# Optimization experiments

Measured on AMD Instinct MI355X. Metric: run time of the kernel, lower is better.

The kernel has to match this reference:

```python
import jax, jax.numpy as jnp
import numpy as np

B, C_IMG, H, W = 16, 512, 32, 32
C_AUD, K_LEN, N_HEADS = 512, 256, 8
HEAD_DIM = C_AUD // N_HEADS
EPS = 1e-5


def setup_inputs() -> dict:
    key = jax.random.key(0)
    ks = jax.random.split(key, 12)
    s_img = 1.0 / np.sqrt(C_IMG)
    s_aud = 1.0 / np.sqrt(C_AUD)
    return {
        "img_feat": jax.random.normal(ks[0], (B, C_IMG, H, W), jnp.float32),
        "audio_feat": jax.random.normal(ks[1], (B, K_LEN, C_AUD), jnp.float32),
        "Wq": jax.random.uniform(ks[2], (C_IMG, C_AUD), jnp.float32, -s_img, s_img),
        "bq": jnp.zeros((C_AUD,), jnp.float32),
        "Wk": jax.random.uniform(ks[3], (C_AUD, C_AUD), jnp.float32, -s_aud, s_aud),
        "bk": jnp.zeros((C_AUD,), jnp.float32),
        "Wv": jax.random.uniform(ks[4], (C_AUD, C_AUD), jnp.float32, -s_aud, s_aud),
        "bv": jnp.zeros((C_AUD,), jnp.float32),
        "Wo": jax.random.uniform(ks[5], (C_AUD, C_IMG), jnp.float32, -s_aud, s_aud),
        "bo": jnp.zeros((C_IMG,), jnp.float32),
        "gamma": jnp.ones((C_IMG,), jnp.float32),
        "beta": jnp.zeros((C_IMG,), jnp.float32),
    }


def reference(img_feat, audio_feat, Wq, bq, Wk, bk, Wv, bv, Wo, bo, gamma, beta):
    b, c, h, w = img_feat.shape
    # b c h w -> b (h w) c
    img_seq = img_feat.reshape(b, c, h * w).transpose(0, 2, 1)
    q = img_seq @ Wq + bq                      # [b, q, C_AUD]
    k = audio_feat @ Wk + bk                   # [b, k, C_AUD]
    v = audio_feat @ Wv + bv
    # split heads: b s (h d) -> b h s d
    def split(x):
        bs, s, _ = x.shape
        return x.reshape(bs, s, N_HEADS, HEAD_DIM).transpose(0, 2, 1, 3)
    qh, kh, vh = split(q), split(k), split(v)
    scale = HEAD_DIM ** -0.5
    scores = jnp.einsum('bhqd,bhkd->bhqk', qh, kh) * scale
    weights = jax.nn.softmax(scores, axis=-1)
    attn = jnp.einsum('bhqk,bhkd->bhqd', weights, vh)
    attn = attn.transpose(0, 2, 1, 3).reshape(b, h * w, C_AUD)
    proj = attn @ Wo + bo                      # [b, q, C_IMG]
    y = img_seq + proj
    mu = jnp.mean(y, axis=-1, keepdims=True)
    var = jnp.mean((y - mu) ** 2, axis=-1, keepdims=True)
    y = (y - mu) * jax.lax.rsqrt(var + EPS) * gamma + beta
    # b (h w) c -> b c h w
    return y.transpose(0, 2, 1).reshape(b, c, h, w)
```

## Files before the change

### kernel.cpp

```cpp
#include <hip/hip_runtime.h>
#include <cstddef>

#define B_SZ 16
#define HW 1024
#define CCH 512
#define K_LEN 256
#define N_HEADS 8
#define EPS 1e-5f

typedef __bf16 bf16;
typedef bf16 bf16x8 __attribute__((ext_vector_type(8)));
typedef bf16 bf16x4 __attribute__((ext_vector_type(4)));
typedef bf16 bf16x2 __attribute__((ext_vector_type(2)));
typedef float f32x4 __attribute__((ext_vector_type(4)));

__device__ __forceinline__ void gl_lds16(const bf16* g, bf16* l) {
    __builtin_amdgcn_global_load_lds(
        (const __attribute__((address_space(1))) void*)g,
        (__attribute__((address_space(3))) void*)l, 16, 0, 0);
}

__global__ __launch_bounds__(256) void transpose_cast_img(
    const float* __restrict__ src, bf16* __restrict__ dst)
{
    const int b  = blockIdx.z;
    const int s0 = blockIdx.x * 64;
    const int c0 = blockIdx.y * 64;
    __shared__ bf16 T[64][72];
    const int tid = threadIdx.x;
    {
        const int r = tid >> 2, cs = (tid & 3) << 4;
        const float* sp = src + ((size_t)b * CCH + c0 + r) * HW + s0 + cs;
        #pragma unroll
        for (int i = 0; i < 4; ++i) {
            float4 f = *(const float4*)(sp + i * 4);
            T[r][cs + i*4 + 0] = (bf16)f.x;
            T[r][cs + i*4 + 1] = (bf16)f.y;
            T[r][cs + i*4 + 2] = (bf16)f.z;
            T[r][cs + i*4 + 3] = (bf16)f.w;
        }
    }
    __syncthreads();
    {
        const int ss = tid >> 2, ks = (tid & 3) << 4;
        bf16x8 a, b8;
        #pragma unroll
        for (int j = 0; j < 8; ++j) { a[j] = T[ks + j][ss]; b8[j] = T[ks + 8 + j][ss]; }
        bf16* dp = dst + ((size_t)b * HW + s0 + ss) * CCH + c0 + ks;
        *(bf16x8*)dp = a;
        *(bf16x8*)(dp + 8) = b8;
    }
}

__global__ __launch_bounds__(256) void transpose_cast_w(
    const float* __restrict__ Wq, const float* __restrict__ Wk,
    const float* __restrict__ Wv, const float* __restrict__ Wo,
    bf16* __restrict__ dst)
{
    const int w = blockIdx.z;
    const float* src = (w == 0) ? Wq : (w == 1) ? Wk : (w == 2) ? Wv : Wo;
    const int n0 = blockIdx.x * 64;
    const int k0 = blockIdx.y * 64;
    __shared__ bf16 T[64][72];
    const int tid = threadIdx.x;
    {
        const int r = tid >> 2, cs = (tid & 3) << 4;
        const float* sp = src + (size_t)(k0 + r) * CCH + n0 + cs;
        #pragma unroll
        for (int i = 0; i < 4; ++i) {
            float4 f = *(const float4*)(sp + i * 4);
            T[r][cs + i*4 + 0] = (bf16)f.x;
            T[r][cs + i*4 + 1] = (bf16)f.y;
            T[r][cs + i*4 + 2] = (bf16)f.z;
            T[r][cs + i*4 + 3] = (bf16)f.w;
        }
    }
    __syncthreads();
    {
        const int nn = tid >> 2, ks = (tid & 3) << 4;
        bf16x8 a, b8;
        #pragma unroll
        for (int j = 0; j < 8; ++j) { a[j] = T[ks + j][nn]; b8[j] = T[ks + 8 + j][nn]; }
        bf16* dp = dst + (size_t)w * CCH * CCH + (size_t)(n0 + nn) * CCH + k0 + ks;
        *(bf16x8*)dp = a;
        *(bf16x8*)(dp + 8) = b8;
    }
}

__global__ __launch_bounds__(256) void cast_audio(
    const float* __restrict__ src, bf16* __restrict__ dst)
{
    const size_t i = ((size_t)blockIdx.x * 256 + threadIdx.x) * 8;
    float4 a = *(const float4*)(src + i);
    float4 b = *(const float4*)(src + i + 4);
    bf16x8 o;
    o[0] = (bf16)a.x; o[1] = (bf16)a.y; o[2] = (bf16)a.z; o[3] = (bf16)a.w;
    o[4] = (bf16)b.x; o[5] = (bf16)b.y; o[6] = (bf16)b.z; o[7] = (bf16)b.w;
    *(bf16x8*)(dst + i) = o;
}

__global__ __launch_bounds__(256) void gemm_bf16_mfma(
    const bf16* __restrict__ A, const bf16* __restrict__ Bt,
    const float* __restrict__ bias, bf16* __restrict__ out)
{
    const int tid  = threadIdx.x;
    const int wave = tid >> 6, lane = tid & 63;
    const int m0 = blockIdx.x * 128;
    const int n0 = blockIdx.y * 128;
    const int l15 = lane & 15, quad = lane >> 4;
    const int wm = (wave >> 1) * 64, wn = (wave & 1) * 64;

    __shared__ bf16 As[128 * 32];
    __shared__ bf16 Bs[128 * 32];

    const int r16 = lane >> 2;
    const int ks  = (lane & 3) * 8;

    f32x4 acc[4][4];
    #pragma unroll
    for (int i = 0; i < 4; ++i)
        #pragma unroll
        for (int j = 0; j < 4; ++j)
            acc[i][j] = (f32x4){0.f, 0.f, 0.f, 0.f};

    for (int k0 = 0; k0 < 512; k0 += 32) {
        #pragma unroll
        for (int i = 0; i < 2; ++i) {
            const int c = wave * 2 + i;
            gl_lds16(A  + (size_t)(m0 + c * 16 + r16) * 512 + k0 + ks, &As[c * 512]);
            gl_lds16(Bt + (size_t)(n0 + c * 16 + r16) * 512 + k0 + ks, &Bs[c * 512]);
        }
        __syncthreads();
        bf16x8 af[4], bfr[4];
        #pragma unroll
        for (int i = 0; i < 4; ++i)
            af[i] = *(const bf16x8*)&As[(wm + i * 16 + l15) * 32 + quad * 8];
        #pragma unroll
        for (int j = 0; j < 4; ++j)
            bfr[j] = *(const bf16x8*)&Bs[(wn + j * 16 + l15) * 32 + quad * 8];
        #pragma unroll
        for (int i = 0; i < 4; ++i)
            #pragma unroll
            for (int j = 0; j < 4; ++j)
                acc[i][j] = __builtin_amdgcn_mfma_f32_16x16x32_bf16(bfr[j], af[i], acc[i][j], 0, 0, 0);
        __syncthreads();
    }

    #pragma unroll
    for (int j = 0; j < 4; ++j) {
        const int gn = n0 + wn + j * 16 + quad * 4;
        const f32x4 bv4 = *(const f32x4*)(bias + gn);
        #pragma unroll
        for (int i = 0; i < 4; ++i) {
            const int gm = m0 + wm + i * 16 + l15;
            bf16x4 ov;
            #pragma unroll
            for (int r = 0; r < 4; ++r) ov[r] = (bf16)(acc[i][j][r] + bv4[r]);
            *(bf16x4*)(out + (size_t)gm * 512 + gn) = ov;
        }
    }
}

__global__ __launch_bounds__(256) void gemm_kv_mfma(
    const bf16* __restrict__ A, const bf16* __restrict__ Bt,
    const float* __restrict__ bk, const float* __restrict__ bv,
    bf16* __restrict__ khout, bf16* __restrict__ vtout)
{
    const int tid  = threadIdx.x;
    const int wave = tid >> 6, lane = tid & 63;
    const int m0 = blockIdx.x * 128;
    const int n0 = blockIdx.y * 128;
    const int l15 = lane & 15, quad = lane >> 4;
    const int wm = (wave >> 1) * 64, wn = (wave & 1) * 64;

    __shared__ bf16 As[128 * 32];
    __shared__ bf16 Bs[128 * 32];

    const int r16 = lane >> 2;
    const int ks  = (lane & 3) * 8;

    f32x4 acc[4][4];
    #pragma unroll
    for (int i = 0; i < 4; ++i)
        #pragma unroll
        for (int j = 0; j < 4; ++j)
            acc[i][j] = (f32x4){0.f, 0.f, 0.f, 0.f};

    for (int k0 = 0; k0 < 512; k0 += 32) {
        #pragma unroll
        for (int i = 0; i < 2; ++i) {
            const int c = wave * 2 + i;
            gl_lds16(A  + (size_t)(m0 + c * 16 + r16) * 512 + k0 + ks, &As[c * 512]);
            gl_lds16(Bt + (size_t)(n0 + c * 16 + r16) * 512 + k0 + ks, &Bs[c * 512]);
        }
        __syncthreads();
        bf16x8 af[4], bfr[4];
        #pragma unroll
        for (int i = 0; i < 4; ++i)
            af[i] = *(const bf16x8*)&As[(wm + i * 16 + l15) * 32 + quad * 8];
        #pragma unroll
        for (int j = 0; j < 4; ++j)
            bfr[j] = *(const bf16x8*)&Bs[(wn + j * 16 + l15) * 32 + quad * 8];
        #pragma unroll
        for (int i = 0; i < 4; ++i)
            #pragma unroll
            for (int j = 0; j < 4; ++j)
                acc[i][j] = __builtin_amdgcn_mfma_f32_16x16x32_bf16(af[i], bfr[j], acc[i][j], 0, 0, 0);
        __syncthreads();
    }

    #pragma unroll
    for (int j = 0; j < 4; ++j) {
        const int gn = n0 + wn + j * 16 + l15;
        if (gn < 512) {
            const int h = gn >> 6, d = gn & 63;
            const float bias = bk[gn];
            #pragma unroll
            for (int i = 0; i < 4; ++i) {
                const int gm = m0 + wm + i * 16 + quad * 4;
                const int b = gm >> 8, key = gm & 255;
                bf16* base = khout + ((((size_t)b * N_HEADS + h) * K_LEN) + key) * 64 + d;
                #pragma unroll
                for (int r = 0; r < 4; ++r)
                    base[(size_t)r * 64] = (bf16)(acc[i][j][r] + bias);
            }
        } else {
            const int ch = gn - 512;
            const int h = ch >> 6, d = ch & 63;
            const float bias = bv[ch];
            #pragma unroll
            for (int i = 0; i < 4; ++i) {
                const int gm = m0 + wm + i * 16 + quad * 4;
                const int b = gm >> 8, key = gm & 255;
                bf16x4 pk;
                #pragma unroll
                for (int r = 0; r < 4; ++r) pk[r] = (bf16)(acc[i][j][r] + bias);
                *(bf16x4*)(vtout + (((size_t)b * N_HEADS + h) * 64 + d) * K_LEN + key) = pk;
            }
        }
    }
}

__global__ __launch_bounds__(256) void attn_mfma(
    const bf16* __restrict__ q,
    const bf16* __restrict__ kh,
    const bf16* __restrict__ vt,
    bf16* __restrict__ o)
{
    const int bh = blockIdx.x;
    const int s0 = blockIdx.y * 64;
    const int tid = threadIdx.x;
    const int wave = tid >> 6, lane = tid & 63;
    const int l15 = lane & 15, quad = lane >> 4;
    const int b = bh >> 3, h = bh & 7;

    __shared__ bf16 KsPt[18432];
    __shared__ bf16 Vs[16896];

    const bf16* khb = kh + (size_t)bh * K_LEN * 64;
    const bf16* vtb = vt + (size_t)bh * 64 * K_LEN;

    #pragma unroll
    for (int i = 0; i < 8; ++i) {
        const int chunk = tid + (i << 8);
        const int key = chunk >> 3, dseg = (chunk & 7) << 3;
        *(bf16x8*)&KsPt[key * 72 + dseg] = *(const bf16x8*)(khb + key * 64 + dseg);
        const int d = chunk >> 5, kseg = (chunk & 31) << 3;
        *(bf16x8*)&Vs[d * 264 + kseg] = *(const bf16x8*)(vtb + d * 256 + kseg);
    }
    __syncthreads();

    const int qrow = s0 + wave * 16 + l15;
    const bf16* qp = q + ((size_t)(b * HW + qrow)) * 512 + h * 64 + quad * 8;
    const bf16x8 qf0 = *(const bf16x8*)qp;
    const bf16x8 qf1 = *(const bf16x8*)(qp + 32);

    f32x4 acc[16];
    #pragma unroll
    for (int m = 0; m < 16; ++m) acc[m] = (f32x4){0.f, 0.f, 0.f, 0.f};
    #pragma unroll
    for (int m = 0; m < 16; ++m) {
        const bf16x8 a0 = *(const bf16x8*)&KsPt[(m * 16 + l15) * 72 + quad * 8];
        const bf16x8 a1 = *(const bf16x8*)&KsPt[(m * 16 + l15) * 72 + 32 + quad * 8];
        acc[m] = __builtin_amdgcn_mfma_f32_16x16x32_bf16(a0, qf0, acc[m], 0, 0, 0);
        acc[m] = __builtin_amdgcn_mfma_f32_16x16x32_bf16(a1, qf1, acc[m], 0, 0, 0);
    }

    float mx = -1e30f;
    #pragma unroll
    for (int m = 0; m < 16; ++m)
        mx = fmaxf(mx, fmaxf(fmaxf(acc[m][0], acc[m][1]), fmaxf(acc[m][2], acc[m][3])));
    mx = fmaxf(mx, __shfl_xor(mx, 16, 64));
    mx = fmaxf(mx, __shfl_xor(mx, 32, 64));

    __syncthreads();

    bf16* PtW = &KsPt[wave * 4224];
    float l_sum = 0.f;
    #pragma unroll
    for (int m = 0; m < 16; ++m) {
        bf16x4 pk;
        #pragma unroll
        for (int r = 0; r < 4; ++r) {
            const float p = __expf((acc[m][r] - mx) * 0.125f);
            l_sum += p;
            pk[r] = (bf16)p;
        }
        *(bf16x4*)&PtW[l15 * 264 + m * 16 + quad * 4] = pk;
    }
    l_sum += __shfl_xor(l_sum, 16, 64);
    l_sum += __shfl_xor(l_sum, 32, 64);
    __syncthreads();

    f32x4 oacc[4];
    #pragma unroll
    for (int m = 0; m < 4; ++m) oacc[m] = (f32x4){0.f, 0.f, 0.f, 0.f};
    #pragma unroll
    for (int s = 0; s < 8; ++s) {
        const bf16x8 pb = *(const bf16x8*)&PtW[l15 * 264 + s * 32 + quad * 8];
        #pragma unroll
        for (int m = 0; m < 4; ++m) {
            const bf16x8 va = *(const bf16x8*)&Vs[(m * 16 + l15) * 264 + s * 32 + quad * 8];
            oacc[m] = __builtin_amdgcn_mfma_f32_16x16x32_bf16(va, pb, oacc[m], 0, 0, 0);
        }
    }

    const float inv = 1.0f / l_sum;
    bf16* op = o + ((size_t)(b * HW + qrow)) * 512 + h * 64 + quad * 4;
    #pragma unroll
    for (int m = 0; m < 4; ++m) {
        bf16x4 ov;
        #pragma unroll
        for (int r = 0; r < 4; ++r) ov[r] = (bf16)(oacc[m][r] * inv);
        *(bf16x4*)&op[m * 16] = ov;
    }
}

__global__ __launch_bounds__(512) void gemm_oln(
    const bf16* __restrict__ A,
    const bf16* __restrict__ Wt,
    const float* __restrict__ bo,
    const bf16* __restrict__ imgb,
    const float* __restrict__ gamma, const float* __restrict__ beta,
    float* __restrict__ out)
{
    const int tid  = threadIdx.x;
    const int wave = tid >> 6, lane = tid & 63;
    const int l15 = lane & 15, quad = lane >> 4;
    const int m0 = blockIdx.x * 64;
    const int b  = m0 >> 10, s0 = m0 & 1023;
    const int wn = wave * 64;

    __shared__ union {
        struct { bf16 As[64 * 32]; bf16 Bs[512 * 32]; } st;
        bf16 Ys[64 * 522];
    } u;
    __shared__ float rsumS[64 * 8];
    __shared__ float rsqS[64 * 8];

    const int r16 = lane >> 2;
    const int ks  = (lane & 3) * 8;

    f32x4 acc[4][4];
    #pragma unroll
    for (int i = 0; i < 4; ++i)
        #pragma unroll
        for (int j = 0; j < 4; ++j)
            acc[i][j] = (f32x4){0.f, 0.f, 0.f, 0.f};

    for (int k0 = 0; k0 < 512; k0 += 32) {
        #pragma unroll
        for (int t = 0; t < 4; ++t) {
            const int cb = wave + (t << 3);
            gl_lds16(Wt + (size_t)(cb * 16 + r16) * 512 + k0 + ks, &u.st.Bs[cb * 512]);
        }
        if (wave < 4)
            gl_lds16(A + (size_t)(m0 + wave * 16 + r16) * 512 + k0 + ks, &u.st.As[wave * 512]);
        __syncthreads();
        bf16x8 af[4], bfr[4];
        #pragma unroll
        for (int i = 0; i < 4; ++i)
            af[i] = *(const bf16x8*)&u.st.As[(i * 16 + l15) * 32 + quad * 8];
        #pragma unroll
        for (int j = 0; j < 4; ++j)
            bfr[j] = *(const bf16x8*)&u.st.Bs[(wn + j * 16 + l15) * 32 + quad * 8];
        #pragma unroll
        for (int i = 0; i < 4; ++i)
            #pragma unroll
            for (int j = 0; j < 4; ++j)
                acc[i][j] = __builtin_amdgcn_mfma_f32_16x16x32_bf16(bfr[j], af[i], acc[i][j], 0, 0, 0);
        __syncthreads();
    }

    float rs_[4] = {0.f, 0.f, 0.f, 0.f};
    float rq_[4] = {0.f, 0.f, 0.f, 0.f};
    #pragma unroll
    for (int j = 0; j < 4; ++j) {
        const int n = wn + j * 16 + quad * 4;
        const f32x4 bo4 = *(const f32x4*)(bo + n);
        #pragma unroll
        for (int i = 0; i < 4; ++i) {
            const int lm = i * 16 + l15;
            const bf16x4 res = *(const bf16x4*)(imgb + (size_t)(m0 + lm) * 512 + n);
            #pragma unroll
            for (int r = 0; r < 4; ++r) {
                const float y = acc[i][j][r] + bo4[r] + (float)res[r];
                acc[i][j][r] = y;
                rs_[i] += y;
                rq_[i] += y * y;
            }
        }
    }
    #pragma unroll
    for (int i = 0; i < 4; ++i) {
        rs_[i] += __shfl_xor(rs_[i], 16, 64);
        rs_[i] += __shfl_xor(rs_[i], 32, 64);
        rq_[i] += __shfl_xor(rq_[i], 16, 64);
        rq_[i] += __shfl_xor(rq_[i], 32, 64);
    }
    if (quad == 0) {
        #pragma unroll
        for (int i = 0; i < 4; ++i) {
            rsumS[(i * 16 + l15) * 8 + wave] = rs_[i];
            rsqS[(i * 16 + l15) * 8 + wave]  = rq_[i];
        }
    }
    __syncthreads();

    float mu[4], rstd[4];
    #pragma unroll
    for (int i = 0; i < 4; ++i) {
        const int lm = i * 16 + l15;
        float s = 0.f, q = 0.f;
        #pragma unroll
        for (int w = 0; w < 8; ++w) { s += rsumS[lm * 8 + w]; q += rsqS[lm * 8 + w]; }
        mu[i] = s * (1.f / 512.f);
        rstd[i] = rsqrtf(q * (1.f / 512.f) - mu[i] * mu[i] + EPS);
    }

    #pragma unroll
    for (int j = 0; j < 4; ++j) {
        const int n = wn + j * 16 + quad * 4;
        const f32x4 g4 = *(const f32x4*)(gamma + n);
        const f32x4 b4 = *(const f32x4*)(beta + n);
        #pragma unroll
        for (int i = 0; i < 4; ++i) {
            const int lm = i * 16 + l15;
            float z[4];
            #pragma unroll
            for (int r = 0; r < 4; ++r)
                z[r] = (acc[i][j][r] - mu[i]) * rstd[i] * g4[r] + b4[r];
            bf16x2 z01, z23;
            z01[0] = (bf16)z[0]; z01[1] = (bf16)z[1];
            z23[0] = (bf16)z[2]; z23[1] = (bf16)z[3];
            *(bf16x2*)&u.Ys[lm * 522 + n]     = z01;
            *(bf16x2*)&u.Ys[lm * 522 + n + 2] = z23;
        }
    }
    __syncthreads();

    float* ob = out + (size_t)b * CCH * HW + s0 + lane;
    #pragma unroll
    for (int it = 0; it < 32; ++it) {
        const int c = wn + it * 2;
        const bf16x2 z2 = *(const bf16x2*)&u.Ys[lane * 522 + c];
        ob[(size_t)c * HW]       = (float)z2[0];
        ob[(size_t)(c + 1) * HW] = (float)z2[1];
    }
}

extern "C" void kernel_launch(void* const* d_in, const int* in_sizes, int n_in,
                              void* d_out, int out_size, void* d_ws, size_t ws_size,
                              hipStream_t stream) {
    const float* img   = (const float*)d_in[0];
    const float* audio = (const float*)d_in[1];
    const float* Wq    = (const float*)d_in[2];
    const float* bq    = (const float*)d_in[3];
    const float* Wk    = (const float*)d_in[4];
    const float* bk    = (const float*)d_in[5];
    const float* Wv    = (const float*)d_in[6];
    const float* bv    = (const float*)d_in[7];
    const float* Wo    = (const float*)d_in[8];
    const float* bo    = (const float*)d_in[9];
    const float* gamma = (const float*)d_in[10];
    const float* beta  = (const float*)d_in[11];

    bf16* wsb    = (bf16*)d_ws;
    bf16* img_bf = wsb;
    bf16* aud_bf = img_bf + 8388608;
    bf16* wT     = aud_bf + 2097152;
    bf16* q_bf   = wT + 1048576;
    bf16* kh_bf  = q_bf + 8388608;
    bf16* vt_bf  = kh_bf + 2097152;
    bf16* a_bf   = vt_bf + 2097152;

    transpose_cast_img<<<dim3(16, 8, 16), 256, 0, stream>>>(img, img_bf);
    cast_audio<<<dim3(1024), 256, 0, stream>>>(audio, aud_bf);
    transpose_cast_w<<<dim3(8, 8, 4), 256, 0, stream>>>(Wq, Wk, Wv, Wo, wT);

    gemm_bf16_mfma<<<dim3(128, 4), 256, 0, stream>>>(img_bf, wT, bq, q_bf);
    gemm_kv_mfma<<<dim3(32, 8), 256, 0, stream>>>(aud_bf, wT + 262144, bk, bv, kh_bf, vt_bf);
    attn_mfma<<<dim3(B_SZ * N_HEADS, HW / 64), 256, 0, stream>>>(q_bf, kh_bf, vt_bf, a_bf);
    gemm_oln<<<dim3(256), 512, 0, stream>>>(a_bf, wT + 3 * 262144, bo, img_bf, gamma, beta, (float*)d_out);
}
```

Before: 202.5 us.

## Fuse audio cast into KV GEMM and restructure output GEMM+LayerNorm epilogue

Drops the separate audio cast kernel: the KV GEMM now loads fp32 audio and converts it to bf16 while staging into shared memory. The output-projection+LayerNorm kernel is restructured to 32-row tiles with 256 threads and 512 blocks. It reads the fp32 image residual directly in channel-major layout and writes float4 results straight to the output, with no LDS transpose buffer. This removes a launch, intermediate traffic and the bf16 residual rounding, but the KV GEMM loses async LDS loads for A, and Wo tiles are reloaded by twice as many blocks.

```diff
diff --git a/kernel.cpp b/kernel.cpp
--- a/kernel.cpp
+++ b/kernel.cpp
@@ -11,7 +11,6 @@
 typedef __bf16 bf16;
 typedef bf16 bf16x8 __attribute__((ext_vector_type(8)));
 typedef bf16 bf16x4 __attribute__((ext_vector_type(4)));
-typedef bf16 bf16x2 __attribute__((ext_vector_type(2)));
 typedef float f32x4 __attribute__((ext_vector_type(4)));
 
 __device__ __forceinline__ void gl_lds16(const bf16* g, bf16* l) {
@@ -87,18 +86,6 @@
     }
 }
 
-__global__ __launch_bounds__(256) void cast_audio(
-    const float* __restrict__ src, bf16* __restrict__ dst)
-{
-    const size_t i = ((size_t)blockIdx.x * 256 + threadIdx.x) * 8;
-    float4 a = *(const float4*)(src + i);
-    float4 b = *(const float4*)(src + i + 4);
-    bf16x8 o;
-    o[0] = (bf16)a.x; o[1] = (bf16)a.y; o[2] = (bf16)a.z; o[3] = (bf16)a.w;
-    o[4] = (bf16)b.x; o[5] = (bf16)b.y; o[6] = (bf16)b.z; o[7] = (bf16)b.w;
-    *(bf16x8*)(dst + i) = o;
-}
-
 __global__ __launch_bounds__(256) void gemm_bf16_mfma(
     const bf16* __restrict__ A, const bf16* __restrict__ Bt,
     const float* __restrict__ bias, bf16* __restrict__ out)
@@ -162,7 +149,8 @@
 }
 
 __global__ __launch_bounds__(256) void gemm_kv_mfma(
-    const bf16* __restrict__ A, const bf16* __restrict__ Bt,
+    const float* __restrict__ audio,
+    const bf16* __restrict__ Bt,
     const float* __restrict__ bk, const float* __restrict__ bv,
     bf16* __restrict__ khout, bf16* __restrict__ vtout)
 {
@@ -190,8 +178,19 @@
         #pragma unroll
         for (int i = 0; i < 2; ++i) {
             const int c = wave * 2 + i;
-            gl_lds16(A  + (size_t)(m0 + c * 16 + r16) * 512 + k0 + ks, &As[c * 512]);
             gl_lds16(Bt + (size_t)(n0 + c * 16 + r16) * 512 + k0 + ks, &Bs[c * 512]);
+        }
+        #pragma unroll
+        for (int i = 0; i < 2; ++i) {
+            const int u = tid + (i << 8);
+            const int r = u >> 2, seg = (u & 3) << 3;
+            const float* ap = audio + (size_t)(m0 + r) * 512 + k0 + seg;
+            f32x4 a0 = *(const f32x4*)ap;
+            f32x4 a1 = *(const f32x4*)(ap + 4);
+            bf16x8 o;
+            #pragma unroll
+            for (int q = 0; q < 4; ++q) { o[q] = (bf16)a0[q]; o[q + 4] = (bf16)a1[q]; }
+            *(bf16x8*)&As[r * 32 + seg] = o;
         }
         __syncthreads();
         bf16x8 af[4], bfr[4];
@@ -336,136 +335,125 @@
     }
 }
 
-__global__ __launch_bounds__(512) void gemm_oln(
+__global__ __launch_bounds__(256) void gemm_oln(
     const bf16* __restrict__ A,
     const bf16* __restrict__ Wt,
     const float* __restrict__ bo,
-    const bf16* __restrict__ imgb,
+    const float* __restrict__ img,
     const float* __restrict__ gamma, const float* __restrict__ beta,
     float* __restrict__ out)
 {
     const int tid  = threadIdx.x;
     const int wave = tid >> 6, lane = tid & 63;
     const int l15 = lane & 15, quad = lane >> 4;
-    const int m0 = blockIdx.x * 64;
+    const int m0 = blockIdx.x * 32;
     const int b  = m0 >> 10, s0 = m0 & 1023;
-    const int wn = wave * 64;
-
-    __shared__ union {
-        struct { bf16 As[64 * 32]; bf16 Bs[512 * 32]; } st;
-        bf16 Ys[64 * 522];
-    } u;
-    __shared__ float rsumS[64 * 8];
-    __shared__ float rsqS[64 * 8];
+    const int wn = wave * 128;
+
+    __shared__ bf16 As[32 * 32];
+    __shared__ bf16 Bs[512 * 32];
+    __shared__ float redS[2][32][4];
 
     const int r16 = lane >> 2;
     const int ks  = (lane & 3) * 8;
 
-    f32x4 acc[4][4];
-    #pragma unroll
-    for (int i = 0; i < 4; ++i)
-        #pragma unroll
-        for (int j = 0; j < 4; ++j)
+    f32x4 acc[2][8];
+    #pragma unroll
+    for (int i = 0; i < 2; ++i)
+        #pragma unroll
+        for (int j = 0; j < 8; ++j)
             acc[i][j] = (f32x4){0.f, 0.f, 0.f, 0.f};
 
     for (int k0 = 0; k0 < 512; k0 += 32) {
         #pragma unroll
-        for (int t = 0; t < 4; ++t) {
-            const int cb = wave + (t << 3);
-            gl_lds16(Wt + (size_t)(cb * 16 + r16) * 512 + k0 + ks, &u.st.Bs[cb * 512]);
-        }
-        if (wave < 4)
-            gl_lds16(A + (size_t)(m0 + wave * 16 + r16) * 512 + k0 + ks, &u.st.As[wave * 512]);
-        __syncthreads();
-        bf16x8 af[4], bfr[4];
-        #pragma unroll
-        for (int i = 0; i < 4; ++i)
-            af[i] = *(const bf16x8*)&u.st.As[(i * 16 + l15) * 32 + quad * 8];
-        #pragma unroll
-        for (int j = 0; j < 4; ++j)
-            bfr[j] = *(const bf16x8*)&u.st.Bs[(wn + j * 16 + l15) * 32 + quad * 8];
-        #pragma unroll
-        for (int i = 0; i < 4; ++i)
-            #pragma unroll
-            for (int j = 0; j < 4; ++j)
-                acc[i][j] = __builtin_amdgcn_mfma_f32_16x16x32_bf16(bfr[j], af[i], acc[i][j], 0, 0, 0);
-        __syncthreads();
-    }
-
-    float rs_[4] = {0.f, 0.f, 0.f, 0.f};
-    float rq_[4] = {0.f, 0.f, 0.f, 0.f};
-    #pragma unroll
-    for (int j = 0; j < 4; ++j) {
-        const int n = wn + j * 16 + quad * 4;
-        const f32x4 bo4 = *(const f32x4*)(bo + n);
-        #pragma unroll
-        for (int i = 0; i < 4; ++i) {
-            const int lm = i * 16 + l15;
-            const bf16x4 res = *(const bf16x4*)(imgb + (size_t)(m0 + lm) * 512 + n);
+        for (int t = 0; t < 8; ++t) {
+            const int cb = wave * 8 + t;
+            gl_lds16(Wt + (size_t)(cb * 16 + r16) * 512 + k0 + ks, &Bs[cb * 512]);
+        }
+        if (wave < 2)
+            gl_lds16(A + (size_t)(m0 + wave * 16 + r16) * 512 + k0 + ks, &As[wave * 512]);
+        __syncthreads();
+        bf16x8 af[2], bfr[8];
+        #pragma unroll
+        for (int i = 0; i < 2; ++i)
+            af[i] = *(const bf16x8*)&As[(i * 16 + l15) * 32 + quad * 8];
+        #pragma unroll
+        for (int j = 0; j < 8; ++j)
+            bfr[j] = *(const bf16x8*)&Bs[(wn + j * 16 + l15) * 32 + quad * 8];
+        #pragma unroll
+        for (int i = 0; i < 2; ++i)
+            #pragma unroll
+            for (int j = 0; j < 8; ++j)
+                acc[i][j] = __builtin_amdgcn_mfma_f32_16x16x32_bf16(af[i], bfr[j], acc[i][j], 0, 0, 0);
+        __syncthreads();
+    }
+
+    float rs_[2][4] = {}, rq_[2][4] = {};
+    #pragma unroll
+    for (int j = 0; j < 8; ++j) {
+        const int c = wn + j * 16 + l15;
+        const float bo_c = bo[c];
+        #pragma unroll
+        for (int i = 0; i < 2; ++i) {
+            const int sb = s0 + i * 16 + quad * 4;
+            const f32x4 res = *(const f32x4*)(img + ((size_t)b * CCH + c) * HW + sb);
             #pragma unroll
             for (int r = 0; r < 4; ++r) {
-                const float y = acc[i][j][r] + bo4[r] + (float)res[r];
+                const float y = acc[i][j][r] + bo_c + res[r];
                 acc[i][j][r] = y;
-                rs_[i] += y;
-                rq_[i] += y * y;
+                rs_[i][r] += y;
+                rq_[i][r] += y * y;
             }
         }
     }
     #pragma unroll
-    for (int i = 0; i < 4; ++i) {
-        rs_[i] += __shfl_xor(rs_[i], 16, 64);
-        rs_[i] += __shfl_xor(rs_[i], 32, 64);
-        rq_[i] += __shfl_xor(rq_[i], 16, 64);
-        rq_[i] += __shfl_xor(rq_[i], 32, 64);
-    }
-    if (quad == 0) {
-        #pragma unroll
-        for (int i = 0; i < 4; ++i) {
-            rsumS[(i * 16 + l15) * 8 + wave] = rs_[i];
-            rsqS[(i * 16 + l15) * 8 + wave]  = rq_[i];
-        }
-    }
-    __syncthreads();
-
-    float mu[4], rstd[4];
-    #pragma unroll
-    for (int i = 0; i < 4; ++i) {
-        const int lm = i * 16 + l15;
-        float s = 0.f, q = 0.f;
-        #pragma unroll
-        for (int w = 0; w < 8; ++w) { s += rsumS[lm * 8 + w]; q += rsqS[lm * 8 + w]; }
-        mu[i] = s * (1.f / 512.f);
-        rstd[i] = rsqrtf(q * (1.f / 512.f) - mu[i] * mu[i] + EPS);
-    }
-
-    #pragma unroll
-    for (int j = 0; j < 4; ++j) {
-        const int n = wn + j * 16 + quad * 4;
-        const f32x4 g4 = *(const f32x4*)(gamma + n);
-        const f32x4 b4 = *(const f32x4*)(beta + n);
-        #pragma unroll
-        for (int i = 0; i < 4; ++i) {
-            const int lm = i * 16 + l15;
-            float z[4];
+    for (int i = 0; i < 2; ++i)
+        #pragma unroll
+        for (int r = 0; r < 4; ++r) {
+            #pragma unroll
+            for (int m = 1; m < 16; m <<= 1) {
+                rs_[i][r] += __shfl_xor(rs_[i][r], m, 64);
+                rq_[i][r] += __shfl_xor(rq_[i][r], m, 64);
+            }
+        }
+    if (l15 == 0) {
+        #pragma unroll
+        for (int i = 0; i < 2; ++i)
+            #pragma unroll
+            for (int r = 0; r < 4; ++r) {
+                redS[0][i * 16 + quad * 4 + r][wave] = rs_[i][r];
+                redS[1][i * 16 + quad * 4 + r][wave] = rq_[i][r];
+            }
+    }
+    __syncthreads();
+
+    float mu[2][4], rstd[2][4];
+    #pragma unroll
+    for (int i = 0; i < 2; ++i)
+        #pragma unroll
+        for (int r = 0; r < 4; ++r) {
+            const int s = i * 16 + quad * 4 + r;
+            const float sm = redS[0][s][0] + redS[0][s][1] + redS[0][s][2] + redS[0][s][3];
+            const float sq = redS[1][s][0] + redS[1][s][1] + redS[1][s][2] + redS[1][s][3];
+            const float m_ = sm * (1.f / 512.f);
+            mu[i][r] = m_;
+            rstd[i][r] = rsqrtf(sq * (1.f / 512.f) - m_ * m_ + EPS);
+        }
+
+    #pragma unroll
+    for (int j = 0; j < 8; ++j) {
+        const int c = wn + j * 16 + l15;
+        const float g_c = gamma[c];
+        const float be_c = beta[c];
+        #pragma unroll
+        for (int i = 0; i < 2; ++i) {
+            const int sb = s0 + i * 16 + quad * 4;
+            f32x4 z;
             #pragma unroll
             for (int r = 0; r < 4; ++r)
-                z[r] = (acc[i][j][r] - mu[i]) * rstd[i] * g4[r] + b4[r];
-            bf16x2 z01, z23;
-            z01[0] = (bf16)z[0]; z01[1] = (bf16)z[1];
-            z23[0] = (bf16)z[2]; z23[1] = (bf16)z[3];
-            *(bf16x2*)&u.Ys[lm * 522 + n]     = z01;
-            *(bf16x2*)&u.Ys[lm * 522 + n + 2] = z23;
-        }
-    }
-    __syncthreads();
-
-    float* ob = out + (size_t)b * CCH * HW + s0 + lane;
-    #pragma unroll
-    for (int it = 0; it < 32; ++it) {
-        const int c = wn + it * 2;
-        const bf16x2 z2 = *(const bf16x2*)&u.Ys[lane * 522 + c];
-        ob[(size_t)c * HW]       = (float)z2[0];
-        ob[(size_t)(c + 1) * HW] = (float)z2[1];
+                z[r] = (acc[i][j][r] - mu[i][r]) * rstd[i][r] * g_c + be_c;
+            *(f32x4*)(out + ((size_t)b * CCH + c) * HW + sb) = z;
+        }
     }
 }
 
@@ -487,19 +475,17 @@
 
     bf16* wsb    = (bf16*)d_ws;
     bf16* img_bf = wsb;
-    bf16* aud_bf = img_bf + 8388608;
-    bf16* wT     = aud_bf + 2097152;
+    bf16* wT     = img_bf + 8388608;
     bf16* q_bf   = wT + 1048576;
     bf16* kh_bf  = q_bf + 8388608;
     bf16* vt_bf  = kh_bf + 2097152;
     bf16* a_bf   = vt_bf + 2097152;
 
     transpose_cast_img<<<dim3(16, 8, 16), 256, 0, stream>>>(img, img_bf);
-    cast_audio<<<dim3(1024), 256, 0, stream>>>(audio, aud_bf);
     transpose_cast_w<<<dim3(8, 8, 4), 256, 0, stream>>>(Wq, Wk, Wv, Wo, wT);
 
     gemm_bf16_mfma<<<dim3(128, 4), 256, 0, stream>>>(img_bf, wT, bq, q_bf);
-    gemm_kv_mfma<<<dim3(32, 8), 256, 0, stream>>>(aud_bf, wT + 262144, bk, bv, kh_bf, vt_bf);
+    gemm_kv_mfma<<<dim3(32, 8), 256, 0, stream>>>(audio, wT + 262144, bk, bv, kh_bf, vt_bf);
     attn_mfma<<<dim3(B_SZ * N_HEADS, HW / 64), 256, 0, stream>>>(q_bf, kh_bf, vt_bf, a_bf);
-    gemm_oln<<<dim3(256), 512, 0, stream>>>(a_bf, wT + 3 * 262144, bo, img_bf, gamma, beta, (float*)d_out);
-}
+    gemm_oln<<<dim3(512), 256, 0, stream>>>(a_bf, wT + 3 * 262144, bo, img, gamma, beta, (float*)d_out);
+}
```

Measured after the change: 204.2 us. About the same (+0.8%).
